# Optimization experiments

Hardware: AMD Instinct MI355X
Metric: run time of the kernel (lower is better)

## Reference

```python
import jax, jax.numpy as jnp
from jax import lax
import numpy as np

N_LAYERS = 4
D_MODEL = 512
EXPAND = 3
D_INNER = EXPAND * D_MODEL  # 1536
D_STATE = 32
D_CONV = 4
DT_RANK = (D_MODEL + 15) // 16  # 32 (mamba default ceil(d_model/16))
BATCH = 1024
N_FEAT = 68
N_RAIN = 4
N_NONRAIN = N_FEAT - N_RAIN  # 64


def setup_inputs() -> dict:
    key = jax.random.key(0)
    ks = iter(jax.random.split(key, 40))

    def w(shape, s=0.02):
        return jax.random.normal(next(ks), shape, dtype=jnp.float32) * s

    inp = {
        'x': jax.random.normal(next(ks), (BATCH, N_FEAT), dtype=jnp.float32),
        # mamba_input_proj: Linear(64 -> d_model)
        'w_in': w((D_MODEL, N_NONRAIN)), 'b_in': jnp.zeros((D_MODEL,), jnp.float32),
        # per-layer LayerNorms
        'ln_g': jnp.ones((N_LAYERS, D_MODEL), jnp.float32),
        'ln_b': jnp.zeros((N_LAYERS, D_MODEL), jnp.float32),
        # Mamba per-layer params (stacked over layers)
        'W_inproj': w((N_LAYERS, 2 * D_INNER, D_MODEL)),
        'conv_w': w((N_LAYERS, D_INNER, D_CONV), 0.1),
        'conv_b': jnp.zeros((N_LAYERS, D_INNER), jnp.float32),
        'W_xproj': w((N_LAYERS, DT_RANK + 2 * D_STATE, D_INNER)),
        'W_dt': w((N_LAYERS, D_INNER, DT_RANK), 0.1),
        'b_dt': w((N_LAYERS, D_INNER), 0.5),
        'A_log': jnp.broadcast_to(jnp.log(jnp.arange(1, D_STATE + 1, dtype=jnp.float32)), (N_LAYERS, D_INNER, D_STATE)) + 0.0,
        'D_skip': jnp.ones((N_LAYERS, D_INNER), jnp.float32),
        'W_outproj': w((N_LAYERS, D_MODEL, D_INNER)),
        # logistic branch: Linear(4 -> 1) + sigmoid
        'w_log': w((1, N_RAIN), 0.1), 'b_log': jnp.zeros((1,), jnp.float32),
        # gate_proj: Linear(1 -> d_model)
        'W_gate': w((D_MODEL, 1), 0.1), 'b_gate': jnp.zeros((D_MODEL,), jnp.float32),
        # output head: Linear(d_model->32), ReLU, Linear(32->1)
        'W_h1': w((32, D_MODEL)), 'b_h1': jnp.zeros((32,), jnp.float32),
        'W_h2': w((1, 32)), 'b_h2': jnp.zeros((1,), jnp.float32),
    }
    return inp


def _layernorm(x, g, b, eps=1e-5):
    mu = x.mean(-1, keepdims=True)
    var = x.var(-1, keepdims=True)
    return (x - mu) * lax.rsqrt(var + eps) * g + b


def _mamba(x, Win, cw, cb, Wx, Wdt, bdt, Alog, Dp, Wout):
    # x: [B, L, d_model]
    B_, L, _ = x.shape
    xz = jnp.einsum('bld,ed->ble', x, Win)           # [B,L,2*d_inner]
    xc, z = jnp.split(xz, 2, axis=-1)
    # causal depthwise conv1d over L
    xt = jnp.pad(xc.transpose(0, 2, 1), ((0, 0), (0, 0), (D_CONV - 1, 0)))
    conv = lax.conv_general_dilated(xt, cw[:, None, :], (1,), 'VALID',
                                    dimension_numbers=('NCH', 'OIH', 'NCH'),
                                    feature_group_count=D_INNER)
    u = jax.nn.silu((conv + cb[None, :, None]).transpose(0, 2, 1))  # [B,L,d_inner]
    x_dbl = jnp.einsum('bld,ed->ble', u, Wx)         # [B,L,dt_rank+2*d_state]
    dt = x_dbl[..., :DT_RANK]
    Bm = x_dbl[..., DT_RANK:DT_RANK + D_STATE]
    Cm = x_dbl[..., DT_RANK + D_STATE:]
    delta = jax.nn.softplus(jnp.einsum('blr,dr->bld', dt, Wdt) + bdt)  # [B,L,d_inner]
    A = -jnp.exp(Alog)                               # [d_inner, d_state]
    dA = jnp.exp(jnp.einsum('bld,dn->bldn', delta, A))
    dBu = jnp.einsum('bld,bln->bldn', delta * u, Bm)

    def step(h, inp):
        dA_t, dBu_t, C_t = inp
        h = dA_t * h + dBu_t                         # [B,d_inner,d_state]
        return h, jnp.einsum('bdn,bn->bd', h, C_t)

    h0 = jnp.zeros((B_, D_INNER, D_STATE), x.dtype)
    _, ys = lax.scan(step, h0, (dA.transpose(1, 0, 2, 3), dBu.transpose(1, 0, 2, 3), Cm.transpose(1, 0, 2)))
    y = ys.transpose(1, 0, 2) + u * Dp               # [B,L,d_inner]
    y = y * jax.nn.silu(z)
    return jnp.einsum('bld,ed->ble', y, Wout)        # [B,L,d_model]


def reference(x, w_in, b_in, ln_g, ln_b, W_inproj, conv_w, conv_b, W_xproj, W_dt, b_dt,
              A_log, D_skip, W_outproj, w_log, b_log, W_gate, b_gate, W_h1, b_h1, W_h2, b_h2):
    rain = x[:, :N_RAIN]
    nonrain = x[:, N_RAIN:]
    h = jax.nn.relu(nonrain @ w_in.T + b_in)[:, None, :]   # [B,1,d_model]
    for l in range(N_LAYERS):
        res = h
        hn = _layernorm(h, ln_g[l], ln_b[l])
        hn = _mamba(hn, W_inproj[l], conv_w[l], conv_b[l], W_xproj[l], W_dt[l], b_dt[l],
                    A_log[l], D_skip[l], W_outproj[l])
        h = res + hn  # dropout is identity in eval mode
    m = h[:, 0, :]
    lg = jax.nn.sigmoid(rain @ w_log.T + b_log)            # [B,1]
    gate = lg @ W_gate.T + b_gate                          # [B,d_model]
    fused = m * gate
    z1 = jax.nn.relu(fused @ W_h1.T + b_h1)
    logits = (z1 @ W_h2.T + b_h2)[:, 0]
    return jax.nn.sigmoid(logits)
```

## Files before the change

kernel.cpp:

```cpp
#include <hip/hip_runtime.h>

typedef unsigned short u16;
typedef short v8s __attribute__((ext_vector_type(8)));
typedef float v4f __attribute__((ext_vector_type(4)));
typedef u16  v4u __attribute__((ext_vector_type(4)));

__device__ __forceinline__ float bf2f(u16 h){ return __uint_as_float(((unsigned)h)<<16); }
__device__ __forceinline__ u16 f2bf(float f){
  unsigned u = __float_as_uint(f);
  u += 0x7FFFu + ((u>>16)&1u);
  return (u16)(u>>16);
}
__device__ __forceinline__ float siluf(float x){ return x/(1.f+__expf(-x)); }
__device__ __forceinline__ float softplusf(float x){
  return (x>15.f) ? x : __logf(1.f+__expf(x));
}

__global__ __launch_bounds__(256) void cvt_kernel(
  const float* __restrict__ s0, const float* __restrict__ s1,
  const float* __restrict__ s2, const float* __restrict__ s3,
  u16* __restrict__ d0, u16* __restrict__ d1,
  u16* __restrict__ d2, u16* __restrict__ d3)
{
  const int c0=6291456, c1=c0+589824, c2=c1+196608, c3=c2+3145728;
  int i4 = (blockIdx.x*256 + threadIdx.x)*4;
  if(i4 >= c3) return;
  const float* src; u16* dst; int off;
  if(i4 < c0){ src=s0; dst=d0; off=i4; }
  else if(i4 < c1){ src=s1; dst=d1; off=i4-c0; }
  else if(i4 < c2){ src=s2; dst=d2; off=i4-c1; }
  else           { src=s3; dst=d3; off=i4-c2; }
  float4 v = *(const float4*)(src+off);
  v4u o = { f2bf(v.x), f2bf(v.y), f2bf(v.z), f2bf(v.w) };
  *(v4u*)(dst+off) = o;
}

__global__ __launch_bounds__(256) void input_kernel(
  const float* __restrict__ x, const float* __restrict__ w,
  const float* __restrict__ bi, float* __restrict__ h)
{
  int idx = blockIdx.x*256 + threadIdx.x;
  int b = idx >> 9, d = idx & 511;
  const float* xr = x + b*68 + 4;
  const float* wr = w + d*64;
  float a = bi[d];
#pragma unroll
  for(int f=0; f<64; f++) a += xr[f]*wr[f];
  h[idx] = fmaxf(a, 0.f);
}

__global__ __launch_bounds__(256) void ln_kernel(
  float* __restrict__ h, const float* __restrict__ pz, int nz,
  const float* __restrict__ g, const float* __restrict__ bta,
  u16* __restrict__ hn)
{
  int row = blockIdx.x;
  int t = threadIdx.x;
  float v0 = h[row*512 + t], v1 = h[row*512 + 256 + t];
  for(int z=0; z<nz; z++){
    v0 += pz[(size_t)z*524288 + row*512 + t];
    v1 += pz[(size_t)z*524288 + row*512 + 256 + t];
  }
  if(nz){ h[row*512+t] = v0; h[row*512+256+t] = v1; }
  float s = v0+v1, s2 = v0*v0 + v1*v1;
#pragma unroll
  for(int off=32; off; off>>=1){ s += __shfl_down(s, off); s2 += __shfl_down(s2, off); }
  __shared__ float red[8];
  int wid = t>>6;
  if((t&63)==0){ red[wid*2]=s; red[wid*2+1]=s2; }
  __syncthreads();
  float mu = (red[0]+red[2]+red[4]+red[6]) * (1.f/512.f);
  float ms = (red[1]+red[3]+red[5]+red[7]) * (1.f/512.f);
  float rstd = rsqrtf(ms - mu*mu + 1e-5f);
  hn[row*512+t]     = f2bf((v0-mu)*rstd*g[t]     + bta[t]);
  hn[row*512+256+t] = f2bf((v1-mu)*rstd*g[t+256] + bta[t+256]);
}

__global__ __launch_bounds__(256) void sdt_kernel(
  const float* __restrict__ xp, u16* __restrict__ dtb, float* __restrict__ sb)
{
  int t = threadIdx.x;
  int row = blockIdx.x*32 + (t>>3);
  int sub = t&7;
  const float* xr = xp + row*96;
  float a = 0.f;
#pragma unroll
  for(int i=0;i<4;i++){
    int n = sub + 8*i;
    float Bn=0.f, Cn=0.f;
#pragma unroll
    for(int z=0;z<8;z++){ Bn += xr[(size_t)z*98304 + 32+n]; Cn += xr[(size_t)z*98304 + 64+n]; }
    a += Bn*Cn;
  }
  a += __shfl_xor(a,1); a += __shfl_xor(a,2); a += __shfl_xor(a,4);
  if(sub==0) sb[row] = a;
#pragma unroll
  for(int i=0;i<4;i++){
    int r = sub + 8*i;
    float d=0.f;
#pragma unroll
    for(int z=0;z<8;z++) d += xr[(size_t)z*98304 + r];
    dtb[row*32+r] = f2bf(d);
  }
}

template<int BM,int BN,int WM,int WN,int MODE>
__global__ __launch_bounds__(256)
void gemm_mfma(const u16* __restrict__ A, int lda,
               const u16* __restrict__ B, int ldb, int Klen,
               const float* __restrict__ p0, const float* __restrict__ p1,
               const float* __restrict__ p2,
               const u16* __restrict__ q0, const u16* __restrict__ q1,
               u16* __restrict__ o16a, u16* __restrict__ o16b,
               float* __restrict__ o32)
{
  constexpr int MI = WM/16, NI = WN/16;
  constexpr int WCOLS = BN/WN;
  constexpr int LDSK = 40;
  constexpr int CA = BM*4, CB = BN*4;
  constexpr int IA = (CA+255)/256, IB = (CB+255)/256;
  static_assert((BM/WM)*(BN/WN) == 4, "4 waves");
  __shared__ u16 As[BM*LDSK];
  __shared__ u16 Bs[BN*LDSK];
  const int tid  = threadIdx.x;
  const int lane = tid & 63, wid = tid >> 6;
  const int wm = wid / WCOLS, wn = wid % WCOLS;
  const int m0 = blockIdx.y*BM, n0 = blockIdx.x*BN;
  const int k0 = blockIdx.z*Klen;
  const int qd = lane>>4, lr = lane&15;

  v4f acc[MI][NI];
#pragma unroll
  for(int i=0;i<MI;i++)
#pragma unroll
    for(int j=0;j<NI;j++) acc[i][j] = v4f{0.f,0.f,0.f,0.f};

  v8s ra[IA], rb[IB];
  auto loadAB = [&](int kk){
#pragma unroll
    for(int i=0;i<IA;i++){ int s = tid + i*256;
      if(CA%256==0 || s<CA){ int r=s>>2, kg=s&3;
        ra[i] = *(const v8s*)(A + (size_t)(m0+r)*lda + (k0+kk) + kg*8); } }
#pragma unroll
    for(int i=0;i<IB;i++){ int s = tid + i*256;
      if(CB%256==0 || s<CB){ int r=s>>2, kg=s&3;
        rb[i] = *(const v8s*)(B + (size_t)(n0+r)*ldb + (k0+kk) + kg*8); } }
  };

  loadAB(0);
  for(int kk=0; kk<Klen; kk+=32){
    __syncthreads();
#pragma unroll
    for(int i=0;i<IA;i++){ int s = tid + i*256;
      if(CA%256==0 || s<CA){ int r=s>>2, kg=s&3;
        *(v8s*)(As + r*LDSK + kg*8) = ra[i]; } }
#pragma unroll
    for(int i=0;i<IB;i++){ int s = tid + i*256;
      if(CB%256==0 || s<CB){ int r=s>>2, kg=s&3;
        *(v8s*)(Bs + r*LDSK + kg*8) = rb[i]; } }
    __syncthreads();
    if(kk+32 < Klen) loadAB(kk+32);
    v8s af[MI], bfv[NI];
#pragma unroll
    for(int i=0;i<MI;i++) af[i]  = *(const v8s*)(As + (wm*WM + i*16 + lr)*LDSK + qd*8);
#pragma unroll
    for(int j=0;j<NI;j++) bfv[j] = *(const v8s*)(Bs + (wn*WN + j*16 + lr)*LDSK + qd*8);
#pragma unroll
    for(int i=0;i<MI;i++)
#pragma unroll
      for(int j=0;j<NI;j++)
        acc[i][j] = __builtin_amdgcn_mfma_f32_16x16x32_bf16(af[i], bfv[j], acc[i][j], 0,0,0);
  }

#pragma unroll
  for(int i=0;i<MI;i++)
#pragma unroll
    for(int j=0;j<NI;j++){
      const int gb0 = m0 + wm*WM + i*16 + qd*4;
      const int ge  = n0 + wn*WN + j*16 + lr;
#pragma unroll
      for(int r=0;r<4;r++){
        const int gb = gb0 + r;
        float val = acc[i][j][r];
        if constexpr (MODE==0){
          if(ge < 1536){
            float t = val * p0[ge*4+3] + p1[ge];
            o16a[(size_t)gb*1536 + ge] = f2bf(siluf(t));
          } else {
            o16b[(size_t)gb*1536 + (ge-1536)] = f2bf(siluf(val));
          }
        } else if constexpr (MODE==1){
          o32[(size_t)blockIdx.z*98304 + (size_t)gb*96 + ge] = val;
        } else if constexpr (MODE==2){
          float delta = softplusf(val + p0[ge]);
          float uu = bf2f(q0[(size_t)gb*1536+ge]);
          float zz = bf2f(q1[(size_t)gb*1536+ge]);
          o16a[(size_t)gb*1536+ge] = f2bf(uu*(delta*p2[gb] + p1[ge])*zz);
        } else {
          o32[(size_t)blockIdx.z*524288 + (size_t)gb*512 + ge] = val;
        }
      }
    }
}

__global__ __launch_bounds__(256) void head_kernel(
  const float* __restrict__ x, const float* __restrict__ h,
  const float* __restrict__ pz,
  const float* __restrict__ wlog, const float* __restrict__ blog,
  const float* __restrict__ wg, const float* __restrict__ bg,
  const float* __restrict__ wh1, const float* __restrict__ bh1,
  const float* __restrict__ wh2, const float* __restrict__ bh2,
  float* __restrict__ out)
{
  int b = blockIdx.x, t = threadIdx.x;
  __shared__ float fused[512];
  __shared__ float part[256];
  __shared__ float z1s[32];
  float lgin = x[b*68+0]*wlog[0] + x[b*68+1]*wlog[1]
             + x[b*68+2]*wlog[2] + x[b*68+3]*wlog[3] + blog[0];
  float lg = 1.f/(1.f+__expf(-lgin));
  for(int d=t; d<512; d+=256){
    float m = h[(size_t)b*512+d]
            + pz[(size_t)0*524288 + b*512 + d]
            + pz[(size_t)1*524288 + b*512 + d]
            + pz[(size_t)2*524288 + b*512 + d];
    fused[d] = m*(lg*wg[d] + bg[d]);
  }
  __syncthreads();
  int j = t&31, c = t>>5;
  float p = 0.f;
#pragma unroll
  for(int i=0;i<64;i++){ int d = c*64+i; p += fused[d]*wh1[j*512+d]; }
  part[t] = p;
  __syncthreads();
  if(t < 32){
    float z = bh1[t];
#pragma unroll
    for(int cc=0; cc<8; cc++) z += part[cc*32+t];
    z1s[t] = fmaxf(z, 0.f);
  }
  __syncthreads();
  if(t==0){
    float lo = bh2[0];
#pragma unroll
    for(int jj=0;jj<32;jj++) lo += z1s[jj]*wh2[jj];
    out[b] = 1.f/(1.f+__expf(-lo));
  }
}

extern "C" void kernel_launch(void* const* d_in, const int* in_sizes, int n_in,
                              void* d_out, int out_size, void* d_ws, size_t ws_size,
                              hipStream_t stream)
{
  const float* x        = (const float*)d_in[0];
  const float* w_in     = (const float*)d_in[1];
  const float* b_in     = (const float*)d_in[2];
  const float* ln_g     = (const float*)d_in[3];
  const float* ln_b     = (const float*)d_in[4];
  const float* W_inproj = (const float*)d_in[5];
  const float* conv_w   = (const float*)d_in[6];
  const float* conv_b   = (const float*)d_in[7];
  const float* W_xproj  = (const float*)d_in[8];
  const float* W_dt     = (const float*)d_in[9];
  const float* b_dt     = (const float*)d_in[10];
  const float* D_skip   = (const float*)d_in[12];
  const float* W_outproj= (const float*)d_in[13];
  const float* w_log    = (const float*)d_in[14];
  const float* b_log    = (const float*)d_in[15];
  const float* W_gate   = (const float*)d_in[16];
  const float* b_gate   = (const float*)d_in[17];
  const float* W_h1     = (const float*)d_in[18];
  const float* b_h1     = (const float*)d_in[19];
  const float* W_h2     = (const float*)d_in[20];
  const float* b_h2     = (const float*)d_in[21];
  float* out = (float*)d_out;
  (void)in_sizes; (void)n_in; (void)out_size; (void)ws_size;

  char* ws = (char*)d_ws;
  size_t off = 0;
  auto alloc = [&](size_t bytes)->char*{
    char* p = ws + off; off = (off + bytes + 255) & ~(size_t)255; return p; };
  u16*   wInB  = (u16*)  alloc(6291456u*2);
  u16*   wXB   = (u16*)  alloc(589824u*2);
  u16*   wDtB  = (u16*)  alloc(196608u*2);
  u16*   wOutB = (u16*)  alloc(3145728u*2);
  float* h     = (float*)alloc(524288u*4);
  u16*   hn    = (u16*)  alloc(524288u*2);
  u16*   u     = (u16*)  alloc(1572864u*2);
  u16*   zs    = (u16*)  alloc(1572864u*2);
  float* xpart = (float*)alloc(8u*98304u*4);
  u16*   dtb   = (u16*)  alloc(32768u*2);
  float* sb    = (float*)alloc(1024u*4);
  u16*   y     = (u16*)  alloc(1572864u*2);
  float* hpart = (float*)alloc(3u*524288u*4);

  cvt_kernel<<<9984,256,0,stream>>>(W_inproj, W_xproj, W_dt, W_outproj,
                                    wInB, wXB, wDtB, wOutB);
  input_kernel<<<2048,256,0,stream>>>(x, w_in, b_in, h);

  for(int l=0;l<4;l++){
    ln_kernel<<<1024,256,0,stream>>>(h, hpart, l?3:0, ln_g+l*512, ln_b+l*512, hn);
    gemm_mfma<64,64,32,32,0><<<dim3(48,16,1),256,0,stream>>>(
      hn, 512, wInB+(size_t)l*1572864, 512, 512,
      conv_w+l*6144, conv_b+l*1536, nullptr, nullptr, nullptr, u, zs, nullptr);
    gemm_mfma<64,96,32,48,1><<<dim3(1,16,8),256,0,stream>>>(
      u, 1536, wXB+(size_t)l*147456, 1536, 192,
      nullptr, nullptr, nullptr, nullptr, nullptr, nullptr, nullptr, xpart);
    sdt_kernel<<<32,256,0,stream>>>(xpart, dtb, sb);
    gemm_mfma<64,64,32,32,2><<<dim3(24,16,1),256,0,stream>>>(
      dtb, 32, wDtB+(size_t)l*49152, 32, 32,
      b_dt+l*1536, D_skip+l*1536, sb, u, zs, y, nullptr, nullptr);
    gemm_mfma<64,64,32,32,3><<<dim3(8,16,3),256,0,stream>>>(
      y, 1536, wOutB+(size_t)l*786432, 1536, 512,
      nullptr, nullptr, nullptr, nullptr, nullptr, nullptr, nullptr, hpart);
  }

  head_kernel<<<1024,256,0,stream>>>(x, h, hpart, w_log, b_log, W_gate, b_gate,
                                     W_h1, b_h1, W_h2, b_h2, out);
}
```

Baseline: 323.9 us.

## Fuse whole forward pass into one cooperative persistent kernel with grid syncs

Replaces the sequence of per-stage launches (weight conversion, input projection, layernorm, four GEMMs per layer, head) with a single cooperative kernel that walks each stage over tiles and separates stages with grid-wide syncs. Weights are read as fp32 and converted to bf16 inside the GEMM tile load, which removes the separate conversion pass. The out-projection now accumulates straight into h with atomics instead of writing split-K partials that the next layernorm sums. The intent is to cut launch overhead and extra passes. In exchange, each stage runs on a fixed grid of 256 or 512 blocks, the x-projection stage keeps only 16 blocks busy, every stage ends in a grid sync, and atomic accumulation order is nondeterministic.

After: 1.092 ms. 237% more time.

```diff
diff --git a/kernel.cpp b/kernel.cpp
--- a/kernel.cpp
+++ b/kernel.cpp
@@ -1,4 +1,6 @@
 #include <hip/hip_runtime.h>
+#include <hip/hip_cooperative_groups.h>
+namespace cg = cooperative_groups;
 
 typedef unsigned short u16;
 typedef short v8s __attribute__((ext_vector_type(8)));
@@ -14,6 +16,238 @@
 __device__ __forceinline__ float siluf(float x){ return x/(1.f+__expf(-x)); }
 __device__ __forceinline__ float softplusf(float x){
   return (x>15.f) ? x : __logf(1.f+__expf(x));
+}
+
+struct Params {
+  const float *x,*w_in,*b_in,*ln_g,*ln_b,*W_inproj,*conv_w,*conv_b,*W_xproj,
+              *W_dt,*b_dt,*D_skip,*W_outproj,*w_log,*b_log,*W_gate,*b_gate,
+              *W_h1,*b_h1,*W_h2,*b_h2;
+  float* out;
+  float* h;
+  u16*   hn;
+  u16*   u;
+  u16*   zs;
+  u16*   dtb;
+  float* sb;
+  u16*   y;
+};
+
+template<int BM,int BN,int WM,int WN,int MODE>
+__device__ __forceinline__ void gemm_tile(
+  const u16* __restrict__ A, int lda,
+  const float* __restrict__ Bw, int ldb,
+  int m0, int n0, int k0, int Klen,
+  u16* As, u16* Bs, float* Ot,
+  const float* __restrict__ p0, const float* __restrict__ p1,
+  const float* __restrict__ p2,
+  const u16* __restrict__ q0, const u16* __restrict__ q1,
+  u16* __restrict__ o16a, u16* __restrict__ o16b, float* __restrict__ o32,
+  u16* __restrict__ dtb, float* __restrict__ sb)
+{
+  constexpr int MI=WM/16, NI=WN/16, WCOLS=BN/WN;
+  constexpr int LDSK=40;
+  constexpr int CA=BM*4;
+  constexpr int CB=BN*8;
+  constexpr int IA=(CA+255)/256, IB=(CB+255)/256;
+  const int tid=threadIdx.x, lane=tid&63, wid=tid>>6;
+  const int wm=wid/WCOLS, wn=wid%WCOLS;
+  const int qd=lane>>4, lr=lane&15;
+
+  v4f acc[MI][NI];
+#pragma unroll
+  for(int i=0;i<MI;i++)
+#pragma unroll
+    for(int j=0;j<NI;j++) acc[i][j]=v4f{0.f,0.f,0.f,0.f};
+
+  v8s ra[IA]; float4 rb[IB];
+  auto loadAB=[&](int kk){
+#pragma unroll
+    for(int i=0;i<IA;i++){ int s=tid+i*256;
+      if(CA%256==0 || s<CA){ int r=s>>2,kg=s&3;
+        ra[i]=*(const v8s*)(A+(size_t)(m0+r)*lda+(k0+kk)+kg*8); } }
+#pragma unroll
+    for(int i=0;i<IB;i++){ int s=tid+i*256;
+      if(CB%256==0 || s<CB){ int r=s>>3,kg=s&7;
+        rb[i]=*(const float4*)(Bw+(size_t)(n0+r)*ldb+(k0+kk)+kg*4); } }
+  };
+
+  loadAB(0);
+  for(int kk=0;kk<Klen;kk+=32){
+    __syncthreads();
+#pragma unroll
+    for(int i=0;i<IA;i++){ int s=tid+i*256;
+      if(CA%256==0 || s<CA){ int r=s>>2,kg=s&3;
+        *(v8s*)(As+r*LDSK+kg*8)=ra[i]; } }
+#pragma unroll
+    for(int i=0;i<IB;i++){ int s=tid+i*256;
+      if(CB%256==0 || s<CB){ int r=s>>3,kg=s&7;
+        v4u pk={ f2bf(rb[i].x), f2bf(rb[i].y), f2bf(rb[i].z), f2bf(rb[i].w) };
+        *(v4u*)(Bs+r*LDSK+kg*4)=pk; } }
+    __syncthreads();
+    if(kk+32<Klen) loadAB(kk+32);
+    v8s af[MI], bfv[NI];
+#pragma unroll
+    for(int i=0;i<MI;i++) af[i]=*(const v8s*)(As+(wm*WM+i*16+lr)*LDSK+qd*8);
+#pragma unroll
+    for(int j=0;j<NI;j++) bfv[j]=*(const v8s*)(Bs+(wn*WN+j*16+lr)*LDSK+qd*8);
+#pragma unroll
+    for(int i=0;i<MI;i++)
+#pragma unroll
+      for(int j=0;j<NI;j++)
+        acc[i][j]=__builtin_amdgcn_mfma_f32_16x16x32_bf16(af[i],bfv[j],acc[i][j],0,0,0);
+  }
+
+  if constexpr(MODE==1){
+#pragma unroll
+    for(int i=0;i<MI;i++)
+#pragma unroll
+      for(int j=0;j<NI;j++){
+        int lr0=wm*WM+i*16+qd*4, lc=wn*WN+j*16+lr;
+#pragma unroll
+        for(int r=0;r<4;r++) Ot[(lr0+r)*97+lc]=acc[i][j][r];
+      }
+    __syncthreads();
+    int r4=tid>>2, sub=tid&3;
+    const float* orow = Ot + r4*97;
+    float s_=0.f;
+#pragma unroll
+    for(int i=0;i<8;i++){ int n=sub*8+i; s_ += orow[32+n]*orow[64+n]; }
+    s_ += __shfl_xor(s_,1); s_ += __shfl_xor(s_,2);
+    if(sub==0) sb[m0+r4]=s_;
+#pragma unroll
+    for(int i=0;i<8;i++){ int c=sub*8+i; dtb[(size_t)(m0+r4)*32+c]=f2bf(orow[c]); }
+  } else {
+#pragma unroll
+    for(int i=0;i<MI;i++)
+#pragma unroll
+      for(int j=0;j<NI;j++){
+        const int gb0=m0+wm*WM+i*16+qd*4;
+        const int ge =n0+wn*WN+j*16+lr;
+#pragma unroll
+        for(int r=0;r<4;r++){
+          const int gb=gb0+r;
+          float val=acc[i][j][r];
+          if constexpr(MODE==0){
+            if(ge<1536){
+              float t=val*p0[ge*4+3]+p1[ge];
+              o16a[(size_t)gb*1536+ge]=f2bf(siluf(t));
+            }else{
+              o16b[(size_t)gb*1536+(ge-1536)]=f2bf(siluf(val));
+            }
+          } else if constexpr(MODE==2){
+            float delta=softplusf(val+p0[ge]);
+            float uu=bf2f(q0[(size_t)gb*1536+ge]);
+            float zz=bf2f(q1[(size_t)gb*1536+ge]);
+            o16a[(size_t)gb*1536+ge]=f2bf(uu*(delta*p2[gb]+p1[ge])*zz);
+          } else {
+            atomicAdd(o32+(size_t)gb*512+ge, val);
+          }
+        }
+      }
+  }
+}
+
+__global__ __launch_bounds__(256,2) void mega_kernel(Params p)
+{
+  cg::grid_group grid = cg::this_grid();
+  __shared__ u16 As[64*40];
+  __shared__ u16 Bs[96*40];
+  __shared__ float Ot[64*97];
+  __shared__ float red[8];
+  __shared__ float fused[512];
+  __shared__ float part[256];
+  __shared__ float z1s[32];
+  const int bid=blockIdx.x, nb=gridDim.x, tid=threadIdx.x;
+
+  for(int idx=bid*256+tid; idx<1024*512; idx+=nb*256){
+    int b=idx>>9, d=idx&511;
+    const float* xr=p.x+b*68+4;
+    const float* wr=p.w_in+d*64;
+    float a=p.b_in[d];
+#pragma unroll
+    for(int f=0;f<64;f++) a+=xr[f]*wr[f];
+    p.h[idx]=fmaxf(a,0.f);
+  }
+  grid.sync();
+
+  for(int l=0;l<4;l++){
+    const float* g=p.ln_g+l*512; const float* bt=p.ln_b+l*512;
+    for(int row=bid; row<1024; row+=nb){
+      __syncthreads();
+      float v0=p.h[row*512+tid], v1=p.h[row*512+256+tid];
+      float s=v0+v1, s2=v0*v0+v1*v1;
+#pragma unroll
+      for(int off=32; off; off>>=1){ s+=__shfl_down(s,off); s2+=__shfl_down(s2,off); }
+      if((tid&63)==0){ red[(tid>>6)*2]=s; red[(tid>>6)*2+1]=s2; }
+      __syncthreads();
+      float mu=(red[0]+red[2]+red[4]+red[6])*(1.f/512.f);
+      float ms=(red[1]+red[3]+red[5]+red[7])*(1.f/512.f);
+      float rstd=rsqrtf(ms-mu*mu+1e-5f);
+      p.hn[row*512+tid]    =f2bf((v0-mu)*rstd*g[tid]    +bt[tid]);
+      p.hn[row*512+256+tid]=f2bf((v1-mu)*rstd*g[tid+256]+bt[tid+256]);
+    }
+    grid.sync();
+    for(int t=bid; t<768; t+=nb){
+      int mt=t/48, nt=t%48;
+      gemm_tile<64,64,32,32,0>(p.hn,512, p.W_inproj+(size_t)l*3072*512,512,
+        mt*64, nt*64, 0, 512, As,Bs,Ot,
+        p.conv_w+l*6144, p.conv_b+l*1536, nullptr, nullptr,nullptr,
+        p.u, p.zs, nullptr, nullptr,nullptr);
+    }
+    grid.sync();
+    for(int t=bid; t<16; t+=nb){
+      gemm_tile<64,96,32,48,1>(p.u,1536, p.W_xproj+(size_t)l*96*1536,1536,
+        t*64, 0, 0, 1536, As,Bs,Ot,
+        nullptr,nullptr,nullptr,nullptr,nullptr,
+        nullptr,nullptr,nullptr, p.dtb, p.sb);
+    }
+    grid.sync();
+    for(int t=bid; t<384; t+=nb){
+      int mt=t/24, nt=t%24;
+      gemm_tile<64,64,32,32,2>(p.dtb,32, p.W_dt+(size_t)l*1536*32,32,
+        mt*64, nt*64, 0, 32, As,Bs,Ot,
+        p.b_dt+l*1536, p.D_skip+l*1536, p.sb, p.u, p.zs,
+        p.y, nullptr, nullptr, nullptr,nullptr);
+    }
+    grid.sync();
+    for(int t=bid; t<512; t+=nb){
+      int z=t&3, nt=(t>>2)&7, mt=t>>5;
+      gemm_tile<64,64,32,32,3>(p.y,1536, p.W_outproj+(size_t)l*512*1536,1536,
+        mt*64, nt*64, z*384, 384, As,Bs,Ot,
+        nullptr,nullptr,nullptr,nullptr,nullptr,
+        nullptr,nullptr, p.h, nullptr,nullptr);
+    }
+    grid.sync();
+  }
+
+  for(int b=bid; b<1024; b+=nb){
+    __syncthreads();
+    float lgin=p.x[b*68+0]*p.w_log[0]+p.x[b*68+1]*p.w_log[1]
+              +p.x[b*68+2]*p.w_log[2]+p.x[b*68+3]*p.w_log[3]+p.b_log[0];
+    float lg=1.f/(1.f+__expf(-lgin));
+    for(int d=tid; d<512; d+=256)
+      fused[d]=p.h[(size_t)b*512+d]*(lg*p.W_gate[d]+p.b_gate[d]);
+    __syncthreads();
+    int j=tid&31, c=tid>>5;
+    float pp=0.f;
+#pragma unroll
+    for(int i=0;i<64;i++){ int d=c*64+i; pp+=fused[d]*p.W_h1[j*512+d]; }
+    part[tid]=pp;
+    __syncthreads();
+    if(tid<32){
+      float z=p.b_h1[tid];
+#pragma unroll
+      for(int cc=0;cc<8;cc++) z+=part[cc*32+tid];
+      z1s[tid]=fmaxf(z,0.f);
+    }
+    __syncthreads();
+    if(tid==0){
+      float lo=p.b_h2[0];
+#pragma unroll
+      for(int jj=0;jj<32;jj++) lo+=z1s[jj]*p.W_h2[jj];
+      p.out[b]=1.f/(1.f+__expf(-lo));
+    }
+  }
 }
 
 __global__ __launch_bounds__(256) void cvt_kernel(
@@ -294,10 +528,28 @@
   u16*   y     = (u16*)  alloc(1572864u*2);
   float* hpart = (float*)alloc(3u*524288u*4);
 
+  Params prm;
+  prm.x=x; prm.w_in=w_in; prm.b_in=b_in; prm.ln_g=ln_g; prm.ln_b=ln_b;
+  prm.W_inproj=W_inproj; prm.conv_w=conv_w; prm.conv_b=conv_b;
+  prm.W_xproj=W_xproj; prm.W_dt=W_dt; prm.b_dt=b_dt; prm.D_skip=D_skip;
+  prm.W_outproj=W_outproj; prm.w_log=w_log; prm.b_log=b_log;
+  prm.W_gate=W_gate; prm.b_gate=b_gate; prm.W_h1=W_h1; prm.b_h1=b_h1;
+  prm.W_h2=W_h2; prm.b_h2=b_h2; prm.out=out;
+  prm.h=h; prm.hn=hn; prm.u=u; prm.zs=zs; prm.dtb=dtb; prm.sb=sb; prm.y=y;
+
+  int maxb = 1;
+  if(hipOccupancyMaxActiveBlocksPerMultiprocessor(&maxb, mega_kernel, 256, 0)
+     != hipSuccess) maxb = 1;
+  int grid = 256 * (maxb >= 2 ? 2 : 1);
+
+  void* kargs[] = { &prm };
+  hipError_t rc = hipLaunchCooperativeKernel((void*)mega_kernel,
+                    dim3(grid), dim3(256), kargs, 0, stream);
+  if(rc == hipSuccess) return;
+
   cvt_kernel<<<9984,256,0,stream>>>(W_inproj, W_xproj, W_dt, W_outproj,
                                     wInB, wXB, wDtB, wOutB);
   input_kernel<<<2048,256,0,stream>>>(x, w_in, b_in, h);
-
   for(int l=0;l<4;l++){
     ln_kernel<<<1024,256,0,stream>>>(h, hpart, l?3:0, ln_g+l*512, ln_b+l*512, hn);
     gemm_mfma<64,64,32,32,0><<<dim3(48,16,1),256,0,stream>>>(
@@ -314,7 +566,6 @@
       y, 1536, wOutB+(size_t)l*786432, 1536, 512,
       nullptr, nullptr, nullptr, nullptr, nullptr, nullptr, nullptr, hpart);
   }
-
   head_kernel<<<1024,256,0,stream>>>(x, h, hpart, w_log, b_log, W_gate, b_gate,
                                      W_h1, b_h1, W_h2, b_h2, out);
 }
```

## Fuse LayerNorm into in-proj GEMM, convert weights on the fly, atomic residual

Applied to the files above, without the earlier changes.

Removes the separate weight-conversion kernel: each GEMM now reads the fp32 weights directly and converts them to bf16 as it stages them into shared memory. LayerNorm is folded into the first GEMM, which computes per-row statistics and normalizes the A tiles on load. The out-projection adds its split-K partials straight into h with atomicAdd, so the partial buffers and their reduction in LN and the head go away. Global loads are now double-buffered two steps ahead. In exchange the weights are read in fp32 at twice the bytes and converted again in every tile, and atomic accumulation makes the floating-point summation order nondeterministic.

New measurement: 377.4 us. +16.5%, slower.

```diff
diff --git a/kernel.cpp b/kernel.cpp
--- a/kernel.cpp
+++ b/kernel.cpp
@@ -16,25 +16,6 @@
   return (x>15.f) ? x : __logf(1.f+__expf(x));
 }
 
-__global__ __launch_bounds__(256) void cvt_kernel(
-  const float* __restrict__ s0, const float* __restrict__ s1,
-  const float* __restrict__ s2, const float* __restrict__ s3,
-  u16* __restrict__ d0, u16* __restrict__ d1,
-  u16* __restrict__ d2, u16* __restrict__ d3)
-{
-  const int c0=6291456, c1=c0+589824, c2=c1+196608, c3=c2+3145728;
-  int i4 = (blockIdx.x*256 + threadIdx.x)*4;
-  if(i4 >= c3) return;
-  const float* src; u16* dst; int off;
-  if(i4 < c0){ src=s0; dst=d0; off=i4; }
-  else if(i4 < c1){ src=s1; dst=d1; off=i4-c0; }
-  else if(i4 < c2){ src=s2; dst=d2; off=i4-c1; }
-  else           { src=s3; dst=d3; off=i4-c2; }
-  float4 v = *(const float4*)(src+off);
-  v4u o = { f2bf(v.x), f2bf(v.y), f2bf(v.z), f2bf(v.w) };
-  *(v4u*)(dst+off) = o;
-}
-
 __global__ __launch_bounds__(256) void input_kernel(
   const float* __restrict__ x, const float* __restrict__ w,
   const float* __restrict__ bi, float* __restrict__ h)
@@ -49,31 +30,181 @@
   h[idx] = fmaxf(a, 0.f);
 }
 
-__global__ __launch_bounds__(256) void ln_kernel(
-  float* __restrict__ h, const float* __restrict__ pz, int nz,
-  const float* __restrict__ g, const float* __restrict__ bta,
-  u16* __restrict__ hn)
-{
-  int row = blockIdx.x;
-  int t = threadIdx.x;
-  float v0 = h[row*512 + t], v1 = h[row*512 + 256 + t];
-  for(int z=0; z<nz; z++){
-    v0 += pz[(size_t)z*524288 + row*512 + t];
-    v1 += pz[(size_t)z*524288 + row*512 + 256 + t];
-  }
-  if(nz){ h[row*512+t] = v0; h[row*512+256+t] = v1; }
-  float s = v0+v1, s2 = v0*v0 + v1*v1;
-#pragma unroll
-  for(int off=32; off; off>>=1){ s += __shfl_down(s, off); s2 += __shfl_down(s2, off); }
-  __shared__ float red[8];
-  int wid = t>>6;
-  if((t&63)==0){ red[wid*2]=s; red[wid*2+1]=s2; }
+__global__ __launch_bounds__(256) void gemm1_ln(
+  const float* __restrict__ h, const float* __restrict__ g,
+  const float* __restrict__ bta, const float* __restrict__ Wip,
+  const float* __restrict__ convw, const float* __restrict__ convb,
+  u16* __restrict__ u, u16* __restrict__ zs)
+{
+  __shared__ u16 As[64*40];
+  __shared__ u16 Bs[64*40];
+  __shared__ float mu_s[64], rs_s[64];
+  __shared__ float gs[512], bs2[512];
+  const int tid=threadIdx.x, lane=tid&63, wid=tid>>6;
+  const int wm=wid>>1, wn=wid&1;
+  const int qd=lane>>4, lr=lane&15;
+  const int m0=blockIdx.y*64, n0=blockIdx.x*64;
+
+  if(tid<128)      ((float4*)gs)[tid]      = ((const float4*)g)[tid];
+  else             ((float4*)bs2)[tid-128] = ((const float4*)bta)[tid-128];
+
+  {
+    int r=tid>>2, q=tid&3;
+    const float4* hr = (const float4*)(h + (size_t)(m0+r)*512 + q*128);
+    float s=0.f, s2=0.f;
+#pragma unroll
+    for(int i=0;i<32;i++){
+      float4 v=hr[i];
+      s += v.x+v.y+v.z+v.w;
+      s2 += v.x*v.x+v.y*v.y+v.z*v.z+v.w*v.w;
+    }
+    s  += __shfl_xor(s,1);  s  += __shfl_xor(s,2);
+    s2 += __shfl_xor(s2,1); s2 += __shfl_xor(s2,2);
+    if(q==0){
+      float mu = s*(1.f/512.f);
+      mu_s[r]=mu;
+      rs_s[r]=rsqrtf(s2*(1.f/512.f) - mu*mu + 1e-5f);
+    }
+  }
   __syncthreads();
-  float mu = (red[0]+red[2]+red[4]+red[6]) * (1.f/512.f);
-  float ms = (red[1]+red[3]+red[5]+red[7]) * (1.f/512.f);
-  float rstd = rsqrtf(ms - mu*mu + 1e-5f);
-  hn[row*512+t]     = f2bf((v0-mu)*rstd*g[t]     + bta[t]);
-  hn[row*512+256+t] = f2bf((v1-mu)*rstd*g[t+256] + bta[t+256]);
+
+  v4f acc[2][2];
+#pragma unroll
+  for(int i=0;i<2;i++)
+#pragma unroll
+    for(int j=0;j<2;j++) acc[i][j]=v4f{0.f,0.f,0.f,0.f};
+
+  float4 raf[2][2], rbf[2][2];
+  auto loadA=[&](int set,int kk){
+#pragma unroll
+    for(int i=0;i<2;i++){ int s=tid+i*256; int r=s>>3, kc=s&7;
+      raf[set][i]=*(const float4*)(h+(size_t)(m0+r)*512+kk+kc*4); }
+  };
+  auto loadB=[&](int set,int kk){
+#pragma unroll
+    for(int i=0;i<2;i++){ int s=tid+i*256; int r=s>>3, kc=s&7;
+      rbf[set][i]=*(const float4*)(Wip+(size_t)(n0+r)*512+kk+kc*4); }
+  };
+  loadA(0,0); loadB(0,0); loadA(1,32); loadB(1,32);
+
+  for(int it=0; it<16; it++){
+    const int kk=it*32, set=it&1;
+    __syncthreads();
+#pragma unroll
+    for(int i=0;i<2;i++){ int s=tid+i*256; int r=s>>3, kc=s&7;
+      float4 v=raf[set][i];
+      float mu=mu_s[r], rs=rs_s[r];
+      int c = kk+kc*4;
+      v4u pk = { f2bf((v.x-mu)*rs*gs[c  ]+bs2[c  ]),
+                 f2bf((v.y-mu)*rs*gs[c+1]+bs2[c+1]),
+                 f2bf((v.z-mu)*rs*gs[c+2]+bs2[c+2]),
+                 f2bf((v.w-mu)*rs*gs[c+3]+bs2[c+3]) };
+      *(v4u*)(As+r*40+kc*4)=pk;
+    }
+#pragma unroll
+    for(int i=0;i<2;i++){ int s=tid+i*256; int r=s>>3, kc=s&7;
+      float4 v=rbf[set][i];
+      v4u pk={ f2bf(v.x), f2bf(v.y), f2bf(v.z), f2bf(v.w) };
+      *(v4u*)(Bs+r*40+kc*4)=pk;
+    }
+    __syncthreads();
+    if(it+2<16){ loadA(set,kk+64); loadB(set,kk+64); }
+    v8s af[2], bfv[2];
+#pragma unroll
+    for(int i=0;i<2;i++) af[i] =*(const v8s*)(As+(wm*32+i*16+lr)*40+qd*8);
+#pragma unroll
+    for(int j=0;j<2;j++) bfv[j]=*(const v8s*)(Bs+(wn*32+j*16+lr)*40+qd*8);
+#pragma unroll
+    for(int i=0;i<2;i++)
+#pragma unroll
+      for(int j=0;j<2;j++)
+        acc[i][j]=__builtin_amdgcn_mfma_f32_16x16x32_bf16(af[i],bfv[j],acc[i][j],0,0,0);
+  }
+
+#pragma unroll
+  for(int i=0;i<2;i++)
+#pragma unroll
+    for(int j=0;j<2;j++){
+      const int gb0=m0+wm*32+i*16+qd*4;
+      const int ge =n0+wn*32+j*16+lr;
+#pragma unroll
+      for(int r=0;r<4;r++){
+        const int gb=gb0+r;
+        float val=acc[i][j][r];
+        if(ge<1536){
+          float t=val*convw[ge*4+3]+convb[ge];
+          u[(size_t)gb*1536+ge]=f2bf(siluf(t));
+        }else{
+          zs[(size_t)gb*1536+(ge-1536)]=f2bf(siluf(val));
+        }
+      }
+    }
+}
+
+__global__ __launch_bounds__(256) void gemm2_k(
+  const u16* __restrict__ A, const float* __restrict__ Bw,
+  float* __restrict__ xpart)
+{
+  __shared__ u16 As[64*40];
+  __shared__ u16 Bs[96*40];
+  const int tid=threadIdx.x, lane=tid&63, wid=tid>>6;
+  const int wm=wid>>1, wn=wid&1;
+  const int qd=lane>>4, lr=lane&15;
+  const int m0=blockIdx.y*64;
+  const int k0=blockIdx.z*192;
+
+  v4f acc[2][3];
+#pragma unroll
+  for(int i=0;i<2;i++)
+#pragma unroll
+    for(int j=0;j<3;j++) acc[i][j]=v4f{0.f,0.f,0.f,0.f};
+
+  v8s ra[2][1]; float4 rb[2][3];
+  auto loadA=[&](int set,int kk){
+    int r=tid>>2, kg=tid&3;
+    ra[set][0]=*(const v8s*)(A+(size_t)(m0+r)*1536+kk+kg*8);
+  };
+  auto loadB=[&](int set,int kk){
+#pragma unroll
+    for(int i=0;i<3;i++){ int s=tid+i*256; int r=s>>3, kc=s&7;
+      rb[set][i]=*(const float4*)(Bw+(size_t)r*1536+kk+kc*4); }
+  };
+  loadA(0,k0); loadB(0,k0); loadA(1,k0+32); loadB(1,k0+32);
+
+  for(int it=0; it<6; it++){
+    const int kk=k0+it*32, set=it&1;
+    __syncthreads();
+    { int r=tid>>2, kg=tid&3; *(v8s*)(As+r*40+kg*8)=ra[set][0]; }
+#pragma unroll
+    for(int i=0;i<3;i++){ int s=tid+i*256; int r=s>>3, kc=s&7;
+      float4 v=rb[set][i];
+      v4u pk={ f2bf(v.x), f2bf(v.y), f2bf(v.z), f2bf(v.w) };
+      *(v4u*)(Bs+r*40+kc*4)=pk;
+    }
+    __syncthreads();
+    if(it+2<6){ loadA(set,kk+64); loadB(set,kk+64); }
+    v8s af[2], bfv[3];
+#pragma unroll
+    for(int i=0;i<2;i++) af[i] =*(const v8s*)(As+(wm*32+i*16+lr)*40+qd*8);
+#pragma unroll
+    for(int j=0;j<3;j++) bfv[j]=*(const v8s*)(Bs+(wn*48+j*16+lr)*40+qd*8);
+#pragma unroll
+    for(int i=0;i<2;i++)
+#pragma unroll
+      for(int j=0;j<3;j++)
+        acc[i][j]=__builtin_amdgcn_mfma_f32_16x16x32_bf16(af[i],bfv[j],acc[i][j],0,0,0);
+  }
+
+#pragma unroll
+  for(int i=0;i<2;i++)
+#pragma unroll
+    for(int j=0;j<3;j++){
+      const int gb0=m0+wm*32+i*16+qd*4;
+      const int ge =wn*48+j*16+lr;
+#pragma unroll
+      for(int r=0;r<4;r++)
+        xpart[(size_t)blockIdx.z*98304+(size_t)(gb0+r)*96+ge]=acc[i][j][r];
+    }
 }
 
 __global__ __launch_bounds__(256) void sdt_kernel(
@@ -104,108 +235,131 @@
   }
 }
 
-template<int BM,int BN,int WM,int WN,int MODE>
-__global__ __launch_bounds__(256)
-void gemm_mfma(const u16* __restrict__ A, int lda,
-               const u16* __restrict__ B, int ldb, int Klen,
-               const float* __restrict__ p0, const float* __restrict__ p1,
-               const float* __restrict__ p2,
-               const u16* __restrict__ q0, const u16* __restrict__ q1,
-               u16* __restrict__ o16a, u16* __restrict__ o16b,
-               float* __restrict__ o32)
-{
-  constexpr int MI = WM/16, NI = WN/16;
-  constexpr int WCOLS = BN/WN;
-  constexpr int LDSK = 40;
-  constexpr int CA = BM*4, CB = BN*4;
-  constexpr int IA = (CA+255)/256, IB = (CB+255)/256;
-  static_assert((BM/WM)*(BN/WN) == 4, "4 waves");
-  __shared__ u16 As[BM*LDSK];
-  __shared__ u16 Bs[BN*LDSK];
-  const int tid  = threadIdx.x;
-  const int lane = tid & 63, wid = tid >> 6;
-  const int wm = wid / WCOLS, wn = wid % WCOLS;
-  const int m0 = blockIdx.y*BM, n0 = blockIdx.x*BN;
-  const int k0 = blockIdx.z*Klen;
-  const int qd = lane>>4, lr = lane&15;
-
-  v4f acc[MI][NI];
-#pragma unroll
-  for(int i=0;i<MI;i++)
-#pragma unroll
-    for(int j=0;j<NI;j++) acc[i][j] = v4f{0.f,0.f,0.f,0.f};
-
-  v8s ra[IA], rb[IB];
-  auto loadAB = [&](int kk){
-#pragma unroll
-    for(int i=0;i<IA;i++){ int s = tid + i*256;
-      if(CA%256==0 || s<CA){ int r=s>>2, kg=s&3;
-        ra[i] = *(const v8s*)(A + (size_t)(m0+r)*lda + (k0+kk) + kg*8); } }
-#pragma unroll
-    for(int i=0;i<IB;i++){ int s = tid + i*256;
-      if(CB%256==0 || s<CB){ int r=s>>2, kg=s&3;
-        rb[i] = *(const v8s*)(B + (size_t)(n0+r)*ldb + (k0+kk) + kg*8); } }
-  };
-
-  loadAB(0);
-  for(int kk=0; kk<Klen; kk+=32){
-    __syncthreads();
-#pragma unroll
-    for(int i=0;i<IA;i++){ int s = tid + i*256;
-      if(CA%256==0 || s<CA){ int r=s>>2, kg=s&3;
-        *(v8s*)(As + r*LDSK + kg*8) = ra[i]; } }
-#pragma unroll
-    for(int i=0;i<IB;i++){ int s = tid + i*256;
-      if(CB%256==0 || s<CB){ int r=s>>2, kg=s&3;
-        *(v8s*)(Bs + r*LDSK + kg*8) = rb[i]; } }
-    __syncthreads();
-    if(kk+32 < Klen) loadAB(kk+32);
-    v8s af[MI], bfv[NI];
-#pragma unroll
-    for(int i=0;i<MI;i++) af[i]  = *(const v8s*)(As + (wm*WM + i*16 + lr)*LDSK + qd*8);
-#pragma unroll
-    for(int j=0;j<NI;j++) bfv[j] = *(const v8s*)(Bs + (wn*WN + j*16 + lr)*LDSK + qd*8);
-#pragma unroll
-    for(int i=0;i<MI;i++)
-#pragma unroll
-      for(int j=0;j<NI;j++)
-        acc[i][j] = __builtin_amdgcn_mfma_f32_16x16x32_bf16(af[i], bfv[j], acc[i][j], 0,0,0);
-  }
-
-#pragma unroll
-  for(int i=0;i<MI;i++)
-#pragma unroll
-    for(int j=0;j<NI;j++){
-      const int gb0 = m0 + wm*WM + i*16 + qd*4;
-      const int ge  = n0 + wn*WN + j*16 + lr;
+__global__ __launch_bounds__(256) void gemm3_k(
+  const u16* __restrict__ A, const float* __restrict__ Bw,
+  const float* __restrict__ bdt, const float* __restrict__ Dp,
+  const float* __restrict__ sb,
+  const u16* __restrict__ u, const u16* __restrict__ zs,
+  u16* __restrict__ y)
+{
+  __shared__ u16 As[64*40];
+  __shared__ u16 Bs[64*40];
+  const int tid=threadIdx.x, lane=tid&63, wid=tid>>6;
+  const int wm=wid>>1, wn=wid&1;
+  const int qd=lane>>4, lr=lane&15;
+  const int m0=blockIdx.y*64, n0=blockIdx.x*64;
+
+  { int r=tid>>2, kg=tid&3;
+    *(v8s*)(As+r*40+kg*8)=*(const v8s*)(A+(size_t)(m0+r)*32+kg*8); }
+#pragma unroll
+  for(int i=0;i<2;i++){ int s=tid+i*256; int r=s>>3, kc=s&7;
+    float4 v=*(const float4*)(Bw+(size_t)(n0+r)*32+kc*4);
+    v4u pk={ f2bf(v.x), f2bf(v.y), f2bf(v.z), f2bf(v.w) };
+    *(v4u*)(Bs+r*40+kc*4)=pk;
+  }
+  __syncthreads();
+
+  v4f acc[2][2];
+#pragma unroll
+  for(int i=0;i<2;i++)
+#pragma unroll
+    for(int j=0;j<2;j++) acc[i][j]=v4f{0.f,0.f,0.f,0.f};
+  v8s af[2], bfv[2];
+#pragma unroll
+  for(int i=0;i<2;i++) af[i] =*(const v8s*)(As+(wm*32+i*16+lr)*40+qd*8);
+#pragma unroll
+  for(int j=0;j<2;j++) bfv[j]=*(const v8s*)(Bs+(wn*32+j*16+lr)*40+qd*8);
+#pragma unroll
+  for(int i=0;i<2;i++)
+#pragma unroll
+    for(int j=0;j<2;j++)
+      acc[i][j]=__builtin_amdgcn_mfma_f32_16x16x32_bf16(af[i],bfv[j],acc[i][j],0,0,0);
+
+#pragma unroll
+  for(int i=0;i<2;i++)
+#pragma unroll
+    for(int j=0;j<2;j++){
+      const int gb0=m0+wm*32+i*16+qd*4;
+      const int ge =n0+wn*32+j*16+lr;
 #pragma unroll
       for(int r=0;r<4;r++){
-        const int gb = gb0 + r;
-        float val = acc[i][j][r];
-        if constexpr (MODE==0){
-          if(ge < 1536){
-            float t = val * p0[ge*4+3] + p1[ge];
-            o16a[(size_t)gb*1536 + ge] = f2bf(siluf(t));
-          } else {
-            o16b[(size_t)gb*1536 + (ge-1536)] = f2bf(siluf(val));
-          }
-        } else if constexpr (MODE==1){
-          o32[(size_t)blockIdx.z*98304 + (size_t)gb*96 + ge] = val;
-        } else if constexpr (MODE==2){
-          float delta = softplusf(val + p0[ge]);
-          float uu = bf2f(q0[(size_t)gb*1536+ge]);
-          float zz = bf2f(q1[(size_t)gb*1536+ge]);
-          o16a[(size_t)gb*1536+ge] = f2bf(uu*(delta*p2[gb] + p1[ge])*zz);
-        } else {
-          o32[(size_t)blockIdx.z*524288 + (size_t)gb*512 + ge] = val;
-        }
+        const int gb=gb0+r;
+        float delta=softplusf(acc[i][j][r]+bdt[ge]);
+        float uu=bf2f(u[(size_t)gb*1536+ge]);
+        float zz=bf2f(zs[(size_t)gb*1536+ge]);
+        y[(size_t)gb*1536+ge]=f2bf(uu*(delta*sb[gb]+Dp[ge])*zz);
       }
+    }
+}
+
+__global__ __launch_bounds__(256) void gemm4_k(
+  const u16* __restrict__ A, const float* __restrict__ Bw,
+  float* __restrict__ h)
+{
+  __shared__ u16 As[64*40];
+  __shared__ u16 Bs[64*40];
+  const int tid=threadIdx.x, lane=tid&63, wid=tid>>6;
+  const int wm=wid>>1, wn=wid&1;
+  const int qd=lane>>4, lr=lane&15;
+  const int m0=blockIdx.y*64, n0=blockIdx.x*64;
+  const int k0=blockIdx.z*512;
+
+  v4f acc[2][2];
+#pragma unroll
+  for(int i=0;i<2;i++)
+#pragma unroll
+    for(int j=0;j<2;j++) acc[i][j]=v4f{0.f,0.f,0.f,0.f};
+
+  v8s ra[2][1]; float4 rb[2][2];
+  auto loadA=[&](int set,int kk){
+    int r=tid>>2, kg=tid&3;
+    ra[set][0]=*(const v8s*)(A+(size_t)(m0+r)*1536+kk+kg*8);
+  };
+  auto loadB=[&](int set,int kk){
+#pragma unroll
+    for(int i=0;i<2;i++){ int s=tid+i*256; int r=s>>3, kc=s&7;
+      rb[set][i]=*(const float4*)(Bw+(size_t)(n0+r)*1536+kk+kc*4); }
+  };
+  loadA(0,k0); loadB(0,k0); loadA(1,k0+32); loadB(1,k0+32);
+
+  for(int it=0; it<16; it++){
+    const int kk=k0+it*32, set=it&1;
+    __syncthreads();
+    { int r=tid>>2, kg=tid&3; *(v8s*)(As+r*40+kg*8)=ra[set][0]; }
+#pragma unroll
+    for(int i=0;i<2;i++){ int s=tid+i*256; int r=s>>3, kc=s&7;
+      float4 v=rb[set][i];
+      v4u pk={ f2bf(v.x), f2bf(v.y), f2bf(v.z), f2bf(v.w) };
+      *(v4u*)(Bs+r*40+kc*4)=pk;
+    }
+    __syncthreads();
+    if(it+2<16){ loadA(set,kk+64); loadB(set,kk+64); }
+    v8s af[2], bfv[2];
+#pragma unroll
+    for(int i=0;i<2;i++) af[i] =*(const v8s*)(As+(wm*32+i*16+lr)*40+qd*8);
+#pragma unroll
+    for(int j=0;j<2;j++) bfv[j]=*(const v8s*)(Bs+(wn*32+j*16+lr)*40+qd*8);
+#pragma unroll
+    for(int i=0;i<2;i++)
+#pragma unroll
+      for(int j=0;j<2;j++)
+        acc[i][j]=__builtin_amdgcn_mfma_f32_16x16x32_bf16(af[i],bfv[j],acc[i][j],0,0,0);
+  }
+
+#pragma unroll
+  for(int i=0;i<2;i++)
+#pragma unroll
+    for(int j=0;j<2;j++){
+      const int gb0=m0+wm*32+i*16+qd*4;
+      const int ge =n0+wn*32+j*16+lr;
+#pragma unroll
+      for(int r=0;r<4;r++)
+        atomicAdd(h+(size_t)(gb0+r)*512+ge, acc[i][j][r]);
     }
 }
 
 __global__ __launch_bounds__(256) void head_kernel(
   const float* __restrict__ x, const float* __restrict__ h,
-  const float* __restrict__ pz,
   const float* __restrict__ wlog, const float* __restrict__ blog,
   const float* __restrict__ wg, const float* __restrict__ bg,
   const float* __restrict__ wh1, const float* __restrict__ bh1,
@@ -219,13 +373,8 @@
   float lgin = x[b*68+0]*wlog[0] + x[b*68+1]*wlog[1]
              + x[b*68+2]*wlog[2] + x[b*68+3]*wlog[3] + blog[0];
   float lg = 1.f/(1.f+__expf(-lgin));
-  for(int d=t; d<512; d+=256){
-    float m = h[(size_t)b*512+d]
-            + pz[(size_t)0*524288 + b*512 + d]
-            + pz[(size_t)1*524288 + b*512 + d]
-            + pz[(size_t)2*524288 + b*512 + d];
-    fused[d] = m*(lg*wg[d] + bg[d]);
-  }
+  for(int d=t; d<512; d+=256)
+    fused[d] = h[(size_t)b*512+d]*(lg*wg[d] + bg[d]);
   __syncthreads();
   int j = t&31, c = t>>5;
   float p = 0.f;
@@ -280,41 +429,29 @@
   size_t off = 0;
   auto alloc = [&](size_t bytes)->char*{
     char* p = ws + off; off = (off + bytes + 255) & ~(size_t)255; return p; };
-  u16*   wInB  = (u16*)  alloc(6291456u*2);
-  u16*   wXB   = (u16*)  alloc(589824u*2);
-  u16*   wDtB  = (u16*)  alloc(196608u*2);
-  u16*   wOutB = (u16*)  alloc(3145728u*2);
   float* h     = (float*)alloc(524288u*4);
-  u16*   hn    = (u16*)  alloc(524288u*2);
   u16*   u     = (u16*)  alloc(1572864u*2);
   u16*   zs    = (u16*)  alloc(1572864u*2);
   float* xpart = (float*)alloc(8u*98304u*4);
   u16*   dtb   = (u16*)  alloc(32768u*2);
   float* sb    = (float*)alloc(1024u*4);
   u16*   y     = (u16*)  alloc(1572864u*2);
-  float* hpart = (float*)alloc(3u*524288u*4);
-
-  cvt_kernel<<<9984,256,0,stream>>>(W_inproj, W_xproj, W_dt, W_outproj,
-                                    wInB, wXB, wDtB, wOutB);
+
   input_kernel<<<2048,256,0,stream>>>(x, w_in, b_in, h);
 
   for(int l=0;l<4;l++){
-    ln_kernel<<<1024,256,0,stream>>>(h, hpart, l?3:0, ln_g+l*512, ln_b+l*512, hn);
-    gemm_mfma<64,64,32,32,0><<<dim3(48,16,1),256,0,stream>>>(
-      hn, 512, wInB+(size_t)l*1572864, 512, 512,
-      conv_w+l*6144, conv_b+l*1536, nullptr, nullptr, nullptr, u, zs, nullptr);
-    gemm_mfma<64,96,32,48,1><<<dim3(1,16,8),256,0,stream>>>(
-      u, 1536, wXB+(size_t)l*147456, 1536, 192,
-      nullptr, nullptr, nullptr, nullptr, nullptr, nullptr, nullptr, xpart);
+    gemm1_ln<<<dim3(48,16),256,0,stream>>>(
+      h, ln_g+l*512, ln_b+l*512, W_inproj+(size_t)l*1572864,
+      conv_w+l*6144, conv_b+l*1536, u, zs);
+    gemm2_k<<<dim3(1,16,8),256,0,stream>>>(
+      u, W_xproj+(size_t)l*147456, xpart);
     sdt_kernel<<<32,256,0,stream>>>(xpart, dtb, sb);
-    gemm_mfma<64,64,32,32,2><<<dim3(24,16,1),256,0,stream>>>(
-      dtb, 32, wDtB+(size_t)l*49152, 32, 32,
-      b_dt+l*1536, D_skip+l*1536, sb, u, zs, y, nullptr, nullptr);
-    gemm_mfma<64,64,32,32,3><<<dim3(8,16,3),256,0,stream>>>(
-      y, 1536, wOutB+(size_t)l*786432, 1536, 512,
-      nullptr, nullptr, nullptr, nullptr, nullptr, nullptr, nullptr, hpart);
-  }
-
-  head_kernel<<<1024,256,0,stream>>>(x, h, hpart, w_log, b_log, W_gate, b_gate,
+    gemm3_k<<<dim3(24,16),256,0,stream>>>(
+      dtb, W_dt+(size_t)l*49152, b_dt+l*1536, D_skip+l*1536, sb, u, zs, y);
+    gemm4_k<<<dim3(8,16,3),256,0,stream>>>(
+      y, W_outproj+(size_t)l*786432, h);
+  }
+
+  head_kernel<<<1024,256,0,stream>>>(x, h, w_log, b_log, W_gate, b_gate,
                                      W_h1, b_h1, W_h2, b_h2, out);
 }
```
